# Optimization experiments

Measured on AMD Instinct MI355X. Metric: run time of the kernel, lower is better.

Reference implementation:

```python
import jax, jax.numpy as jnp
import numpy as np

B, S, D, H = 2, 2048, 1024, 16
DH = D // H
DIM_K = 1024


def setup_inputs() -> dict:
    key = jax.random.key(0)
    ks = jax.random.split(key, 5)
    sc = 0.02
    return {
        "x": jax.random.normal(ks[0], (B, S, D), dtype=jnp.float32),
        "Wq": jax.random.normal(ks[1], (D, DIM_K), dtype=jnp.float32) * sc,
        "Wk": jax.random.normal(ks[2], (D, DIM_K), dtype=jnp.float32) * sc,
        "Wv": jax.random.normal(ks[3], (D, DIM_K), dtype=jnp.float32) * sc,
        "Wo": jax.random.normal(ks[4], (DIM_K, DIM_K), dtype=jnp.float32) * sc,
    }


def reference(x, Wq, Wk, Wv, Wo):
    # projections (Linear, no bias); weights stored as [in, out]
    q = (x @ Wq).reshape(B, S, H, DH).transpose(0, 2, 1, 3)  # [B,H,S,DH]
    k = (x @ Wk).reshape(B, S, H, DH).transpose(0, 2, 1, 3)
    v = (x @ Wv).reshape(B, S, H, DH).transpose(0, 2, 1, 3)

    scores = jnp.einsum("bhqd,bhkd->bhqk", q, k)  # [B,H,S,S]
    # causal mask applied BEFORE scaling, as in the original
    causal_mask = jnp.triu(jnp.ones((S, S), dtype=bool), k=1)
    m_inf = -jnp.finfo(scores.dtype).max
    scores = jnp.where(causal_mask[None, None], m_inf, scores)
    attn = jax.nn.softmax(scores * (DIM_K ** -0.5), axis=-1)

    out = jnp.einsum("bhqk,bhkd->bhqd", attn, v)  # [B,H,S,DH]
    out = out.transpose(0, 2, 1, 3).reshape(B, S, DIM_K)
    return out @ Wo
```

## Files before the change

### kernel.cpp

```cpp
#include <hip/hip_runtime.h>


#define AS1 __attribute__((address_space(1)))
#define AS3 __attribute__((address_space(3)))
#define EXPC2 0.04508422f

typedef __attribute__((ext_vector_type(4))) float f32x4;
typedef __attribute__((ext_vector_type(8))) short bf16x8;

__device__ __forceinline__ void gload16(const void* g, void* l) {
  __builtin_amdgcn_global_load_lds((const AS1 unsigned int*)g,
                                   (AS3 unsigned int*)l, 16, 0, 0);
}
__device__ __forceinline__ unsigned short f2b(float f) {
  unsigned u = __float_as_uint(f);
  return (unsigned short)((u + 0x7FFFu + ((u >> 16) & 1u)) >> 16);
}
__device__ __forceinline__ float fexp2(float x) {
  float r;
  asm("v_exp_f32 %0, %1" : "=v"(r) : "v"(x));
  return r;
}
__device__ __forceinline__ unsigned cvtpk(float a, float b) {
  unsigned r;
  asm("v_cvt_pk_bf16_f32 %0, %1, %2" : "=v"(r) : "v"(a), "v"(b));
  return r;
}

__global__ __launch_bounds__(256) void prep(
    const float* __restrict__ x, const float* __restrict__ W0,
    const float* __restrict__ W1, const float* __restrict__ W2,
    const float* __restrict__ W3, unsigned short* __restrict__ xb,
    unsigned short* __restrict__ Wt) {
  __shared__ float T[64][65];
  const int tid = threadIdx.x;
  const int bid = blockIdx.x;
  if (bid < 4096) {
    const size_t i = (size_t)(bid * 256 + tid) * 4;
    float4 v = *(const float4*)&x[i];
    uint2 o;
    o.x = f2b(v.x) | ((unsigned)f2b(v.y) << 16);
    o.y = f2b(v.z) | ((unsigned)f2b(v.w) << 16);
    *(uint2*)&xb[i] = o;
    return;
  }
  const int idx = bid - 4096;
  const int kb = (idx & 15) * 64, nb = ((idx >> 4) & 15) * 64, z = idx >> 8;
  const float* W = (z == 0) ? W0 : (z == 1) ? W1 : (z == 2) ? W2 : W3;
  unsigned short* D = Wt + (size_t)z * 1024 * 1024;
#pragma unroll
  for (int p = 0; p < 4; ++p) {
    const int s = p * 256 + tid;
    const int r = s >> 4, c4 = s & 15;
    float4 v = *(const float4*)&W[(size_t)(kb + r) * 1024 + nb + c4 * 4];
    T[r][c4 * 4 + 0] = v.x;
    T[r][c4 * 4 + 1] = v.y;
    T[r][c4 * 4 + 2] = v.z;
    T[r][c4 * 4 + 3] = v.w;
  }
  __syncthreads();
#pragma unroll
  for (int p = 0; p < 4; ++p) {
    const int s = p * 256 + tid;
    const int n = s >> 4, k4 = s & 15;
    uint2 o;
    o.x = f2b(T[k4 * 4 + 0][n]) | ((unsigned)f2b(T[k4 * 4 + 1][n]) << 16);
    o.y = f2b(T[k4 * 4 + 2][n]) | ((unsigned)f2b(T[k4 * 4 + 3][n]) << 16);
    *(uint2*)&D[(size_t)(nb + n) * 1024 + kb + k4 * 4] = o;
  }
}

template <int KIND>
__global__ __launch_bounds__(256) void gemm2ph(
    const unsigned short* __restrict__ A, const unsigned short* __restrict__ B,
    unsigned short* __restrict__ Qb, unsigned short* __restrict__ Kb,
    unsigned short* __restrict__ Vp, float* __restrict__ Of) {
  __shared__ unsigned short smem[16896];

  const int tid = threadIdx.x, lane = tid & 63, w = tid >> 6;
  int bm, bn;
  if constexpr (KIND == 0) {
    bm = blockIdx.x / 24;
    bn = blockIdx.x % 24;
  } else {
    bm = blockIdx.x >> 3;
    bn = blockIdx.x & 7;
  }
  const int wr = w >> 1, wc = w & 1;

  f32x4 acc[4][4];
#pragma unroll
  for (int m = 0; m < 4; ++m)
#pragma unroll
    for (int n = 0; n < 4; ++n) acc[m][n] = (f32x4)0.0f;

  const int lu = (lane & 7) ^ (lane >> 3);
  const int srow2 = 2 * (lane >> 3) + (lu >> 2);
  const int scol2 = (lu & 3) * 8;
  const size_t arow = (size_t)(bm * 128 + srow2) * 1024 + scol2;
  const size_t brow = (size_t)(bn * 128 + srow2) * 1024 + scol2;

  const int fr = lane & 15, g = lane >> 4;
  const int fh = fr >> 1;
  const int pcx = ((((fr & 1) << 2) | g) ^ fh) * 8;

#define GSTAGE(BUF, KC)                                                      \
  {                                                                          \
    _Pragma("unroll") for (int q = 0; q < 2; ++q) {                          \
      const int r = w * 32 + q * 16;                                         \
      gload16(&A[arow + (size_t)r * 1024 + (KC)],                            \
              &smem[(BUF) * 8192 + r * 32]);                                 \
      gload16(&B[brow + (size_t)r * 1024 + (KC)],                            \
              &smem[(BUF) * 8192 + 4096 + r * 32]);                          \
    }                                                                        \
  }

  GSTAGE(0, 0)
  int cur = 0;

  for (int t = 0; t < 32; ++t) {
    __syncthreads();
    if (t + 1 < 32) GSTAGE(cur ^ 1, (t + 1) * 32)

    bf16x8 af[4], bf[4];
#pragma unroll
    for (int m = 0; m < 4; ++m)
      af[m] = *(const bf16x8*)&smem[cur * 8192 + (wr * 32 + m * 8 + fh) * 64 +
                                    pcx];
#pragma unroll
    for (int n = 0; n < 4; ++n)
      bf[n] = *(const bf16x8*)&smem[cur * 8192 + 4096 +
                                    (wc * 32 + n * 8 + fh) * 64 + pcx];
#pragma unroll
    for (int m = 0; m < 4; ++m)
#pragma unroll
      for (int n = 0; n < 4; ++n)
        acc[m][n] = __builtin_amdgcn_mfma_f32_16x16x32_bf16(af[m], bf[n],
                                                            acc[m][n], 0, 0, 0);
    cur ^= 1;
  }

  const int fq = lane >> 4;
  if constexpr (KIND == 1) {
#pragma unroll
    for (int mf = 0; mf < 4; ++mf)
#pragma unroll
      for (int nf = 0; nf < 4; ++nf) {
        const int col = bn * 128 + wc * 64 + nf * 16 + fr;
#pragma unroll
        for (int rr = 0; rr < 4; ++rr) {
          const int m = bm * 128 + wr * 64 + mf * 16 + fq * 4 + rr;
          Of[(size_t)m * 1024 + col] = acc[mf][nf][rr];
        }
      }
    return;
  } else if (bn < 16) {
    unsigned short* Ob = (bn < 8) ? Qb : Kb;
    const int cbase = (bn & 7) * 128;
#pragma unroll
    for (int mf = 0; mf < 4; ++mf)
#pragma unroll
      for (int nf = 0; nf < 4; ++nf) {
        const int col = cbase + wc * 64 + nf * 16 + fr;
        const int h = col >> 6, d = col & 63;
#pragma unroll
        for (int rr = 0; rr < 4; ++rr) {
          const int m = bm * 128 + wr * 64 + mf * 16 + fq * 4 + rr;
          const int b = m >> 11, s = m & 2047;
          Ob[((size_t)(b * 16 + h) * 2048 + s) * 64 + d] = f2b(acc[mf][nf][rr]);
        }
      }
    return;
  }

  __syncthreads();
#pragma unroll
  for (int mf = 0; mf < 4; ++mf)
#pragma unroll
    for (int nf = 0; nf < 4; ++nf) {
      const int cl = wc * 64 + nf * 16 + fr;
#pragma unroll
      for (int rr = 0; rr < 4; ++rr) {
        const int ml = wr * 64 + mf * 16 + fq * 4 + rr;
        const int u = ml & 63, a = u >> 4;
        const int sperm = (ml & 64) | ((a >> 1) * 32 + ((u >> 2) & 3) * 8 +
                                       (a & 1) * 4 + (u & 3));
        smem[cl * 132 + sperm] = f2b(acc[mf][nf][rr]);
      }
    }
  __syncthreads();
  const int l5 = lane & 31;
  const size_t sbase = (size_t)((bm * 128) & 2047);
  const int bV = bm >> 4;
#pragma unroll
  for (int it = 0; it < 16; ++it) {
    const int rl = w * 32 + it * 2 + (lane >> 5);
    const int rowg = (bn - 16) * 128 + rl;
    const int h = rowg >> 6, d = rowg & 63;
    uint2 v = *(const uint2*)&smem[rl * 132 + l5 * 4];
    *(uint2*)&Vp[((size_t)(bV * 16 + h) * 64 + d) * 2048 + sbase + l5 * 4] = v;
  }
#undef GSTAGE
}

__global__ __launch_bounds__(256) void attn_q64(
    const unsigned short* __restrict__ Qb, const unsigned short* __restrict__ Kb,
    const unsigned short* __restrict__ Vp, unsigned short* __restrict__ Ab) {
  __shared__ unsigned short smem[16384];

  const int tid = threadIdx.x, lane = tid & 63, w = tid >> 6;
  const int lo = lane & 15, hi = lane >> 4;

  const int id = blockIdx.x;
  const int qtr = id >> 8;
  const int g = (id >> 5) & 7;
  const int bh = id & 31;
  const int bq = (qtr == 0)   ? 2 * g
                 : (qtr == 1) ? 2 * g + 1
                 : (qtr == 2) ? 31 - 2 * g
                              : 30 - 2 * g;
  const int qw = bq * 64 + w * 16;
  const size_t base = (size_t)bh * (2048 * 64);

  bf16x8 qf[2];
#pragma unroll
  for (int ks = 0; ks < 2; ++ks)
    qf[ks] =
        *(const bf16x8*)&Qb[base + (size_t)(qw + lo) * 64 + ks * 32 + hi * 8];

  f32x4 accO[4];
#pragma unroll
  for (int mf = 0; mf < 4; ++mf) accO[mf] = (f32x4)0.0f;
  float mrow = -1e30f, lpart = 0.0f;

  const int ntile = bq + 1;
  const unsigned short* kgb = Kb + base;
  const unsigned short* vgb = Vp + base;
  const int lseg = w * 512;

#define STAGE(BUF, KBASE)                                                    \
  {                                                                          \
    const int kb_ = (KBASE);                                                 \
    _Pragma("unroll") for (int qq = 0; qq < 2; ++qq) {                       \
      const int slot = qq * 256 + tid;                                       \
      const int row = slot >> 3, ch = (slot & 7) ^ (row & 7);                \
      gload16(kgb + (size_t)(kb_ + row) * 64 + ch * 8,                       \
              &smem[(BUF)*4096 + qq * 2048 + lseg]);                         \
      gload16(vgb + (size_t)row * 2048 + kb_ + ch * 8,                       \
              &smem[8192 + (BUF)*4096 + qq * 2048 + lseg]);                  \
    }                                                                        \
  }

  STAGE(0, 0)
  int cur = 0;

  for (int t = 0; t < ntile; ++t) {
    __syncthreads();
    if (t + 1 < ntile) STAGE(cur ^ 1, (t + 1) * 64)

    const int kb = t * 64;
    const int x7 = lo & 7;
    bf16x8 ka[2][4];
#pragma unroll
    for (int ks = 0; ks < 2; ++ks) {
      const int ch = (ks * 4 + hi) ^ x7;
#pragma unroll
      for (int kf = 0; kf < 4; ++kf)
        ka[ks][kf] =
            *(const bf16x8*)&smem[cur * 4096 + (kf * 16 + lo) * 64 + ch * 8];
    }
    f32x4 st[4];
#pragma unroll
    for (int kf = 0; kf < 4; ++kf) st[kf] = (f32x4)0.0f;
    __builtin_amdgcn_s_setprio(1);
#pragma unroll
    for (int ks = 0; ks < 2; ++ks)
#pragma unroll
      for (int kf = 0; kf < 4; ++kf)
        st[kf] = __builtin_amdgcn_mfma_f32_16x16x32_bf16(ka[ks][kf], qf[ks],
                                                         st[kf], 0, 0, 0);
    __builtin_amdgcn_s_setprio(0);

    bf16x8 va[2][4];
#pragma unroll
    for (int ks = 0; ks < 2; ++ks) {
      const int ch = (ks * 4 + hi) ^ x7;
#pragma unroll
      for (int mf = 0; mf < 4; ++mf)
        va[ks][mf] = *(const bf16x8*)&smem[8192 + cur * 4096 +
                                           (mf * 16 + lo) * 64 + ch * 8];
    }

    float v[16];
#pragma unroll
    for (int kf = 0; kf < 4; ++kf)
#pragma unroll
      for (int rr = 0; rr < 4; ++rr) v[kf * 4 + rr] = st[kf][rr];
    if (kb + 63 > qw) {
      const int qg = qw + lo;
#pragma unroll
      for (int kf = 0; kf < 4; ++kf)
#pragma unroll
        for (int rr = 0; rr < 4; ++rr)
          if (kb + kf * 16 + hi * 4 + rr > qg) v[kf * 4 + rr] = -1e30f;
    }
    float mx = fmaxf(fmaxf(fmaxf(v[0], v[1]), fmaxf(v[2], v[3])),
                     fmaxf(fmaxf(v[4], v[5]), fmaxf(v[6], v[7])));
    mx = fmaxf(mx, fmaxf(fmaxf(fmaxf(v[8], v[9]), fmaxf(v[10], v[11])),
                         fmaxf(fmaxf(v[12], v[13]), fmaxf(v[14], v[15]))));
    mx = fmaxf(mx, __shfl_xor(mx, 16));
    mx = fmaxf(mx, __shfl_xor(mx, 32));
    if (!__all(mx - mrow <= 64.0f)) {
      const float mnew = fmaxf(mrow, mx);
      const float al = fexp2((mrow - mnew) * EXPC2);
      mrow = mnew;
      lpart *= al;
#pragma unroll
      for (int mf = 0; mf < 4; ++mf)
#pragma unroll
        for (int rr = 0; rr < 4; ++rr) accO[mf][rr] *= al;
    }
    float p[16], rs = 0.0f;
#pragma unroll
    for (int i = 0; i < 16; ++i) {
      p[i] = fexp2((v[i] - mrow) * EXPC2);
      rs += p[i];
    }
    lpart += rs;

    bf16x8 pb[2];
#pragma unroll
    for (int ks = 0; ks < 2; ++ks) {
      uint4 u;
      u.x = cvtpk(p[ks * 8 + 0], p[ks * 8 + 1]);
      u.y = cvtpk(p[ks * 8 + 2], p[ks * 8 + 3]);
      u.z = cvtpk(p[ks * 8 + 4], p[ks * 8 + 5]);
      u.w = cvtpk(p[ks * 8 + 6], p[ks * 8 + 7]);
      pb[ks] = *(bf16x8*)&u;
    }

    __builtin_amdgcn_s_setprio(1);
#pragma unroll
    for (int ks = 0; ks < 2; ++ks)
#pragma unroll
      for (int mf = 0; mf < 4; ++mf)
        accO[mf] = __builtin_amdgcn_mfma_f32_16x16x32_bf16(va[ks][mf], pb[ks],
                                                           accO[mf], 0, 0, 0);
    __builtin_amdgcn_s_setprio(0);
    cur ^= 1;
  }

  __syncthreads();

  float l = lpart;
  l += __shfl_xor(l, 16);
  l += __shfl_xor(l, 32);
  const float linv = 1.0f / l;
  unsigned short* ot = &smem[w * 1152];
#pragma unroll
  for (int mf = 0; mf < 4; ++mf) {
    uint2 u;
    u.x = cvtpk(accO[mf][0] * linv, accO[mf][1] * linv);
    u.y = cvtpk(accO[mf][2] * linv, accO[mf][3] * linv);
    *(uint2*)&ot[lo * 72 + mf * 16 + hi * 4] = u;
  }
  const int b = bh >> 4, h = bh & 15;
  const int row = lane >> 2, cg = (lane & 3) * 16;
  uint4 o0 = *(const uint4*)&ot[row * 72 + cg];
  uint4 o1 = *(const uint4*)&ot[row * 72 + cg + 8];
  unsigned short* op = &Ab[(size_t)(b * 2048 + qw + row) * 1024 + h * 64 + cg];
  *(uint4*)op = o0;
  *(uint4*)(op + 8) = o1;
}

extern "C" void kernel_launch(void* const* d_in, const int* in_sizes, int n_in,
                              void* d_out, int out_size, void* d_ws,
                              size_t ws_size, hipStream_t stream) {
  (void)in_sizes; (void)n_in; (void)out_size; (void)ws_size;
  const float* x = (const float*)d_in[0];
  const float* Wq = (const float*)d_in[1];
  const float* Wk = (const float*)d_in[2];
  const float* Wv = (const float*)d_in[3];
  const float* Wo = (const float*)d_in[4];
  float* out = (float*)d_out;

  char* ws = (char*)d_ws;
  unsigned short* xb = (unsigned short*)(ws);
  unsigned short* Wt = (unsigned short*)(ws + (8u << 20));
  unsigned short* Qb = (unsigned short*)(ws + (16u << 20));
  unsigned short* Kb = (unsigned short*)(ws + (24u << 20));
  unsigned short* Vp = (unsigned short*)(ws + (32u << 20));
  unsigned short* Ab = (unsigned short*)(ws + (40u << 20));
  unsigned short* Wto = Wt + (size_t)3 * 1024 * 1024;

  prep<<<dim3(5120), 256, 0, stream>>>(x, Wq, Wk, Wv, Wo, xb, Wt);
  gemm2ph<0><<<dim3(768), 256, 0, stream>>>(xb, Wt, Qb, Kb, Vp, nullptr);
  attn_q64<<<dim3(1024), 256, 0, stream>>>(Qb, Kb, Vp, Ab);
  gemm2ph<1><<<dim3(256), 256, 0, stream>>>(Ab, Wto, nullptr, nullptr, nullptr,
                                            out);
}
```

Measured before the change: 111.8 us.

## Drop LDS staging in attention and GEMM A operand, load fragments from global

The attention kernel no longer stages K/V tiles through shared memory. Each wave loads its K and V MFMA fragments straight from global memory, double-buffering K in registers. It now covers 32 query rows per wave in two 16-row halves, and blocks are remapped so each XCD handles a fixed set of heads, with half as many blocks launched. The projection GEMM also loads its A fragments directly from global into registers with register double-buffering, and only B goes through LDS. This removes LDS traffic and barriers but relies on cache hits for data shared across waves, and raises register pressure.

```diff
diff --git a/kernel.cpp b/kernel.cpp
--- a/kernel.cpp
+++ b/kernel.cpp
@@ -97,47 +97,49 @@
   const int lu = (lane & 7) ^ (lane >> 3);
   const int srow2 = 2 * (lane >> 3) + (lu >> 2);
   const int scol2 = (lu & 3) * 8;
-  const size_t arow = (size_t)(bm * 128 + srow2) * 1024 + scol2;
   const size_t brow = (size_t)(bn * 128 + srow2) * 1024 + scol2;
 
   const int fr = lane & 15, g = lane >> 4;
   const int fh = fr >> 1;
   const int pcx = ((((fr & 1) << 2) | g) ^ fh) * 8;
+
+  const size_t aFragBase = (size_t)(bm * 128 + wr * 64 + fr) * 1024 + g * 8;
+  bf16x8 afA[4], afB[4];
+#pragma unroll
+  for (int m = 0; m < 4; ++m)
+    afA[m] = *(const bf16x8*)&A[aFragBase + (size_t)m * 16384];
 
 #define GSTAGE(BUF, KC)                                                      \
   {                                                                          \
     _Pragma("unroll") for (int q = 0; q < 2; ++q) {                          \
       const int r = w * 32 + q * 16;                                         \
-      gload16(&A[arow + (size_t)r * 1024 + (KC)],                            \
-              &smem[(BUF) * 8192 + r * 32]);                                 \
       gload16(&B[brow + (size_t)r * 1024 + (KC)],                            \
-              &smem[(BUF) * 8192 + 4096 + r * 32]);                          \
+              &smem[(BUF) * 4096 + r * 32]);                                 \
     }                                                                        \
   }
 
+#define GSTEP(T, AC, AN)                                                     \
+  {                                                                          \
+    __syncthreads();          \
+    if ((T) + 1 < 32) {                                                      \
+      GSTAGE(((T) + 1) & 1, ((T) + 1) * 32)                                  \
+      _Pragma("unroll") for (int m = 0; m < 4; ++m) AN[m] =                  \
+          *(const bf16x8*)&A[aFragBase + (size_t)m * 16384 + ((T) + 1) * 32];\
+    }                                                                        \
+    bf16x8 bf[4];                                                            \
+    _Pragma("unroll") for (int n = 0; n < 4; ++n) bf[n] =                    \
+        *(const bf16x8*)&smem[((T)&1) * 4096 + (wc * 32 + n * 8 + fh) * 64 + \
+                              pcx];                                          \
+    _Pragma("unroll") for (int m = 0; m < 4; ++m)                            \
+        _Pragma("unroll") for (int n = 0; n < 4; ++n) acc[m][n] =            \
+            __builtin_amdgcn_mfma_f32_16x16x32_bf16(AC[m], bf[n], acc[m][n], \
+                                                    0, 0, 0);                \
+  }
+
   GSTAGE(0, 0)
-  int cur = 0;
-
-  for (int t = 0; t < 32; ++t) {
-    __syncthreads();
-    if (t + 1 < 32) GSTAGE(cur ^ 1, (t + 1) * 32)
-
-    bf16x8 af[4], bf[4];
-#pragma unroll
-    for (int m = 0; m < 4; ++m)
-      af[m] = *(const bf16x8*)&smem[cur * 8192 + (wr * 32 + m * 8 + fh) * 64 +
-                                    pcx];
-#pragma unroll
-    for (int n = 0; n < 4; ++n)
-      bf[n] = *(const bf16x8*)&smem[cur * 8192 + 4096 +
-                                    (wc * 32 + n * 8 + fh) * 64 + pcx];
-#pragma unroll
-    for (int m = 0; m < 4; ++m)
-#pragma unroll
-      for (int n = 0; n < 4; ++n)
-        acc[m][n] = __builtin_amdgcn_mfma_f32_16x16x32_bf16(af[m], bf[n],
-                                                            acc[m][n], 0, 0, 0);
-    cur ^= 1;
+  for (int t = 0; t < 32; t += 2) {
+    GSTEP(t, afA, afB)
+    GSTEP(t + 1, afB, afA)
   }
 
   const int fq = lane >> 4;
@@ -200,177 +202,149 @@
     uint2 v = *(const uint2*)&smem[rl * 132 + l5 * 4];
     *(uint2*)&Vp[((size_t)(bV * 16 + h) * 64 + d) * 2048 + sbase + l5 * 4] = v;
   }
+#undef GSTEP
 #undef GSTAGE
 }
 
-__global__ __launch_bounds__(256) void attn_q64(
+__global__ __launch_bounds__(256) void attn_nolds(
     const unsigned short* __restrict__ Qb, const unsigned short* __restrict__ Kb,
     const unsigned short* __restrict__ Vp, unsigned short* __restrict__ Ab) {
-  __shared__ unsigned short smem[16384];
-
   const int tid = threadIdx.x, lane = tid & 63, w = tid >> 6;
   const int lo = lane & 15, hi = lane >> 4;
 
   const int id = blockIdx.x;
-  const int qtr = id >> 8;
-  const int g = (id >> 5) & 7;
-  const int bh = id & 31;
-  const int bq = (qtr == 0)   ? 2 * g
-                 : (qtr == 1) ? 2 * g + 1
-                 : (qtr == 2) ? 31 - 2 * g
-                              : 30 - 2 * g;
-  const int qw = bq * 64 + w * 16;
+  const int xcd = id & 7, mm = id >> 3;
+  const int bh = xcd * 4 + (mm & 3);
+  const int h8 = mm >> 2;
+  const int bq4 = (h8 < 8) ? h8 : 23 - h8;
+  const int t32 = bq4 * 4 + w;
+  const int qw = t32 * 32;
+  const int ntile = (t32 >> 1) + 1;
   const size_t base = (size_t)bh * (2048 * 64);
-
-  bf16x8 qf[2];
-#pragma unroll
-  for (int ks = 0; ks < 2; ++ks)
-    qf[ks] =
-        *(const bf16x8*)&Qb[base + (size_t)(qw + lo) * 64 + ks * 32 + hi * 8];
-
-  f32x4 accO[4];
-#pragma unroll
-  for (int mf = 0; mf < 4; ++mf) accO[mf] = (f32x4)0.0f;
-  float mrow = -1e30f, lpart = 0.0f;
-
-  const int ntile = bq + 1;
-  const unsigned short* kgb = Kb + base;
-  const unsigned short* vgb = Vp + base;
-  const int lseg = w * 512;
-
-#define STAGE(BUF, KBASE)                                                    \
+  const unsigned short* kg = Kb + base;
+  const unsigned short* vg = Vp + base;
+
+  bf16x8 qf[2][2];
+#pragma unroll
+  for (int qn = 0; qn < 2; ++qn)
+#pragma unroll
+    for (int ks = 0; ks < 2; ++ks)
+      qf[qn][ks] = *(const bf16x8*)&Qb[base +
+                                       (size_t)(qw + qn * 16 + lo) * 64 +
+                                       ks * 32 + hi * 8];
+
+  f32x4 accO[4][2];
+#pragma unroll
+  for (int mf = 0; mf < 4; ++mf)
+#pragma unroll
+    for (int qn = 0; qn < 2; ++qn) accO[mf][qn] = (f32x4)0.0f;
+  float mrow[2] = {-1e30f, -1e30f}, lpart[2] = {0.0f, 0.0f};
+
+  bf16x8 kaA[2][4], kaB[2][4];
+#define LOADK(DST, KB_)                                                      \
+  _Pragma("unroll") for (int ks = 0; ks < 2; ++ks)                           \
+      _Pragma("unroll") for (int kf = 0; kf < 4; ++kf) DST[ks][kf] =         \
+          *(const bf16x8*)&kg[(size_t)((KB_) + kf * 16 + lo) * 64 +          \
+                              ks * 32 + hi * 8];
+
+#define ATILE(T, KA, KN)                                                     \
   {                                                                          \
-    const int kb_ = (KBASE);                                                 \
-    _Pragma("unroll") for (int qq = 0; qq < 2; ++qq) {                       \
-      const int slot = qq * 256 + tid;                                       \
-      const int row = slot >> 3, ch = (slot & 7) ^ (row & 7);                \
-      gload16(kgb + (size_t)(kb_ + row) * 64 + ch * 8,                       \
-              &smem[(BUF)*4096 + qq * 2048 + lseg]);                         \
-      gload16(vgb + (size_t)row * 2048 + kb_ + ch * 8,                       \
-              &smem[8192 + (BUF)*4096 + qq * 2048 + lseg]);                  \
+    const int kb = (T) * 64;                                                 \
+    f32x4 st[4][2];                                                          \
+    _Pragma("unroll") for (int kf = 0; kf < 4; ++kf)                         \
+        _Pragma("unroll") for (int qn = 0; qn < 2; ++qn) st[kf][qn] =        \
+            (f32x4)0.0f;                                                     \
+    __builtin_amdgcn_s_setprio(1);                                           \
+    _Pragma("unroll") for (int ks = 0; ks < 2; ++ks)                         \
+        _Pragma("unroll") for (int kf = 0; kf < 4; ++kf)                     \
+            _Pragma("unroll") for (int qn = 0; qn < 2; ++qn) st[kf][qn] =    \
+                __builtin_amdgcn_mfma_f32_16x16x32_bf16(                     \
+                    KA[ks][kf], qf[qn][ks], st[kf][qn], 0, 0, 0);            \
+    __builtin_amdgcn_s_setprio(0);                                           \
+    if ((T) + 1 < ntile) LOADK(KN, ((T) + 1) * 64)                           \
+    bf16x8 va[2][4];    \
+    _Pragma("unroll") for (int ks = 0; ks < 2; ++ks)                         \
+        _Pragma("unroll") for (int mf = 0; mf < 4; ++mf) va[ks][mf] =        \
+            *(const bf16x8*)&vg[(size_t)(mf * 16 + lo) * 2048 + kb +         \
+                                ks * 32 + hi * 8];                           \
+    bf16x8 pb[2][2];                                                         \
+    _Pragma("unroll") for (int qn = 0; qn < 2; ++qn) {                       \
+      float v[16];                                                           \
+      _Pragma("unroll") for (int kf = 0; kf < 4; ++kf)                       \
+          _Pragma("unroll") for (int rr = 0; rr < 4; ++rr) v[kf * 4 + rr] =  \
+              st[kf][qn][rr];                                                \
+      if (kb + 63 > qw) {                                                    \
+        const int qg = qw + qn * 16 + lo;                                    \
+        _Pragma("unroll") for (int kf = 0; kf < 4; ++kf)                     \
+            _Pragma("unroll") for (int rr = 0; rr < 4; ++rr) if (kb +        \
+                kf * 16 + hi * 4 + rr > qg) v[kf * 4 + rr] = -1e30f;         \
+      }                                                                      \
+      float mx = fmaxf(fmaxf(fmaxf(v[0], v[1]), fmaxf(v[2], v[3])),          \
+                       fmaxf(fmaxf(v[4], v[5]), fmaxf(v[6], v[7])));         \
+      mx = fmaxf(mx, fmaxf(fmaxf(fmaxf(v[8], v[9]), fmaxf(v[10], v[11])),    \
+                           fmaxf(fmaxf(v[12], v[13]), fmaxf(v[14], v[15]))));\
+      mx = fmaxf(mx, __shfl_xor(mx, 16));                                    \
+      mx = fmaxf(mx, __shfl_xor(mx, 32));                                    \
+      if (!__all(mx - mrow[qn] <= 64.0f)) {           \
+        const float mnew = fmaxf(mrow[qn], mx);                              \
+        const float al = fexp2((mrow[qn] - mnew) * EXPC2);                   \
+        mrow[qn] = mnew;                                                     \
+        lpart[qn] *= al;                                                     \
+        _Pragma("unroll") for (int mf = 0; mf < 4; ++mf)                     \
+            _Pragma("unroll") for (int rr = 0; rr < 4; ++rr)                 \
+                accO[mf][qn][rr] *= al;                                      \
+      }                                                                      \
+      float p[16], rs = 0.0f;                                                \
+      _Pragma("unroll") for (int i = 0; i < 16; ++i) {                       \
+        p[i] = fexp2((v[i] - mrow[qn]) * EXPC2);                             \
+        rs += p[i];                                                          \
+      }                                                                      \
+      lpart[qn] += rs;                                                       \
+      _Pragma("unroll") for (int ks = 0; ks < 2; ++ks) {                     \
+        uint4 u;                                                             \
+        u.x = cvtpk(p[ks * 8 + 0], p[ks * 8 + 1]);                           \
+        u.y = cvtpk(p[ks * 8 + 2], p[ks * 8 + 3]);                           \
+        u.z = cvtpk(p[ks * 8 + 4], p[ks * 8 + 5]);                           \
+        u.w = cvtpk(p[ks * 8 + 6], p[ks * 8 + 7]);                           \
+        pb[qn][ks] = *(bf16x8*)&u;                                           \
+      }                                                                      \
     }                                                                        \
-  }
-
-  STAGE(0, 0)
-  int cur = 0;
-
-  for (int t = 0; t < ntile; ++t) {
-    __syncthreads();
-    if (t + 1 < ntile) STAGE(cur ^ 1, (t + 1) * 64)
-
-    const int kb = t * 64;
-    const int x7 = lo & 7;
-    bf16x8 ka[2][4];
-#pragma unroll
-    for (int ks = 0; ks < 2; ++ks) {
-      const int ch = (ks * 4 + hi) ^ x7;
-#pragma unroll
-      for (int kf = 0; kf < 4; ++kf)
-        ka[ks][kf] =
-            *(const bf16x8*)&smem[cur * 4096 + (kf * 16 + lo) * 64 + ch * 8];
+    __builtin_amdgcn_s_setprio(1);                                           \
+    _Pragma("unroll") for (int ks = 0; ks < 2; ++ks)                         \
+        _Pragma("unroll") for (int mf = 0; mf < 4; ++mf)                     \
+            _Pragma("unroll") for (int qn = 0; qn < 2; ++qn) accO[mf][qn] =  \
+                __builtin_amdgcn_mfma_f32_16x16x32_bf16(                     \
+                    va[ks][mf], pb[qn][ks], accO[mf][qn], 0, 0, 0);          \
+    __builtin_amdgcn_s_setprio(0);                                           \
+  }
+
+  LOADK(kaA, 0)
+  int t = 0;
+  while (true) {
+    ATILE(t, kaA, kaB)
+    if (++t >= ntile) break;
+    ATILE(t, kaB, kaA)
+    if (++t >= ntile) break;
+  }
+
+  const int b = bh >> 4, h = bh & 15;
+#pragma unroll
+  for (int qn = 0; qn < 2; ++qn) {
+    float l = lpart[qn];
+    l += __shfl_xor(l, 16);
+    l += __shfl_xor(l, 32);
+    const float linv = 1.0f / l;
+#pragma unroll
+    for (int mf = 0; mf < 4; ++mf) {
+      uint2 u;
+      u.x = cvtpk(accO[mf][qn][0] * linv, accO[mf][qn][1] * linv);
+      u.y = cvtpk(accO[mf][qn][2] * linv, accO[mf][qn][3] * linv);
+      *(uint2*)&Ab[(size_t)(b * 2048 + qw + qn * 16 + lo) * 1024 + h * 64 +
+                   mf * 16 + hi * 4] = u;
     }
-    f32x4 st[4];
-#pragma unroll
-    for (int kf = 0; kf < 4; ++kf) st[kf] = (f32x4)0.0f;
-    __builtin_amdgcn_s_setprio(1);
-#pragma unroll
-    for (int ks = 0; ks < 2; ++ks)
-#pragma unroll
-      for (int kf = 0; kf < 4; ++kf)
-        st[kf] = __builtin_amdgcn_mfma_f32_16x16x32_bf16(ka[ks][kf], qf[ks],
-                                                         st[kf], 0, 0, 0);
-    __builtin_amdgcn_s_setprio(0);
-
-    bf16x8 va[2][4];
-#pragma unroll
-    for (int ks = 0; ks < 2; ++ks) {
-      const int ch = (ks * 4 + hi) ^ x7;
-#pragma unroll
-      for (int mf = 0; mf < 4; ++mf)
-        va[ks][mf] = *(const bf16x8*)&smem[8192 + cur * 4096 +
-                                           (mf * 16 + lo) * 64 + ch * 8];
-    }
-
-    float v[16];
-#pragma unroll
-    for (int kf = 0; kf < 4; ++kf)
-#pragma unroll
-      for (int rr = 0; rr < 4; ++rr) v[kf * 4 + rr] = st[kf][rr];
-    if (kb + 63 > qw) {
-      const int qg = qw + lo;
-#pragma unroll
-      for (int kf = 0; kf < 4; ++kf)
-#pragma unroll
-        for (int rr = 0; rr < 4; ++rr)
-          if (kb + kf * 16 + hi * 4 + rr > qg) v[kf * 4 + rr] = -1e30f;
-    }
-    float mx = fmaxf(fmaxf(fmaxf(v[0], v[1]), fmaxf(v[2], v[3])),
-                     fmaxf(fmaxf(v[4], v[5]), fmaxf(v[6], v[7])));
-    mx = fmaxf(mx, fmaxf(fmaxf(fmaxf(v[8], v[9]), fmaxf(v[10], v[11])),
-                         fmaxf(fmaxf(v[12], v[13]), fmaxf(v[14], v[15]))));
-    mx = fmaxf(mx, __shfl_xor(mx, 16));
-    mx = fmaxf(mx, __shfl_xor(mx, 32));
-    if (!__all(mx - mrow <= 64.0f)) {
-      const float mnew = fmaxf(mrow, mx);
-      const float al = fexp2((mrow - mnew) * EXPC2);
-      mrow = mnew;
-      lpart *= al;
-#pragma unroll
-      for (int mf = 0; mf < 4; ++mf)
-#pragma unroll
-        for (int rr = 0; rr < 4; ++rr) accO[mf][rr] *= al;
-    }
-    float p[16], rs = 0.0f;
-#pragma unroll
-    for (int i = 0; i < 16; ++i) {
-      p[i] = fexp2((v[i] - mrow) * EXPC2);
-      rs += p[i];
-    }
-    lpart += rs;
-
-    bf16x8 pb[2];
-#pragma unroll
-    for (int ks = 0; ks < 2; ++ks) {
-      uint4 u;
-      u.x = cvtpk(p[ks * 8 + 0], p[ks * 8 + 1]);
-      u.y = cvtpk(p[ks * 8 + 2], p[ks * 8 + 3]);
-      u.z = cvtpk(p[ks * 8 + 4], p[ks * 8 + 5]);
-      u.w = cvtpk(p[ks * 8 + 6], p[ks * 8 + 7]);
-      pb[ks] = *(bf16x8*)&u;
-    }
-
-    __builtin_amdgcn_s_setprio(1);
-#pragma unroll
-    for (int ks = 0; ks < 2; ++ks)
-#pragma unroll
-      for (int mf = 0; mf < 4; ++mf)
-        accO[mf] = __builtin_amdgcn_mfma_f32_16x16x32_bf16(va[ks][mf], pb[ks],
-                                                           accO[mf], 0, 0, 0);
-    __builtin_amdgcn_s_setprio(0);
-    cur ^= 1;
-  }
-
-  __syncthreads();
-
-  float l = lpart;
-  l += __shfl_xor(l, 16);
-  l += __shfl_xor(l, 32);
-  const float linv = 1.0f / l;
-  unsigned short* ot = &smem[w * 1152];
-#pragma unroll
-  for (int mf = 0; mf < 4; ++mf) {
-    uint2 u;
-    u.x = cvtpk(accO[mf][0] * linv, accO[mf][1] * linv);
-    u.y = cvtpk(accO[mf][2] * linv, accO[mf][3] * linv);
-    *(uint2*)&ot[lo * 72 + mf * 16 + hi * 4] = u;
-  }
-  const int b = bh >> 4, h = bh & 15;
-  const int row = lane >> 2, cg = (lane & 3) * 16;
-  uint4 o0 = *(const uint4*)&ot[row * 72 + cg];
-  uint4 o1 = *(const uint4*)&ot[row * 72 + cg + 8];
-  unsigned short* op = &Ab[(size_t)(b * 2048 + qw + row) * 1024 + h * 64 + cg];
-  *(uint4*)op = o0;
-  *(uint4*)(op + 8) = o1;
+  }
+#undef ATILE
+#undef LOADK
 }
 
 extern "C" void kernel_launch(void* const* d_in, const int* in_sizes, int n_in,
@@ -395,7 +369,7 @@
 
   prep<<<dim3(5120), 256, 0, stream>>>(x, Wq, Wk, Wv, Wo, xb, Wt);
   gemm2ph<0><<<dim3(768), 256, 0, stream>>>(xb, Wt, Qb, Kb, Vp, nullptr);
-  attn_q64<<<dim3(1024), 256, 0, stream>>>(Qb, Kb, Vp, Ab);
+  attn_nolds<<<dim3(512), 256, 0, stream>>>(Qb, Kb, Vp, Ab);
   gemm2ph<1><<<dim3(256), 256, 0, stream>>>(Ab, Wto, nullptr, nullptr, nullptr,
                                             out);
 }
```

Measured after the change: 179.3 us. +60.5%, slower.

## Split attention across block-tiled kernel and new single-wave register kernel per batch

Applied to the files above, without the earlier changes.

The existing LDS-based attention kernel now handles only the first 16 batch-head pairs. A new single-wave kernel, which reads K and V straight from global memory into registers with double-buffered K fragments, handles the other 16. Each wave computes 32 query rows, and the heaviest tiles are scheduled first. The goal is to try a different occupancy and memory-access structure, but the two kernels run serially on the same stream, and the new one gives up LDS reuse across waves.

```diff
diff --git a/kernel.cpp b/kernel.cpp
--- a/kernel.cpp
+++ b/kernel.cpp
@@ -212,9 +212,9 @@
   const int lo = lane & 15, hi = lane >> 4;
 
   const int id = blockIdx.x;
-  const int qtr = id >> 8;
-  const int g = (id >> 5) & 7;
-  const int bh = id & 31;
+  const int qtr = id >> 7;
+  const int g = (id >> 4) & 7;
+  const int bh = id & 15;
   const int bq = (qtr == 0)   ? 2 * g
                  : (qtr == 1) ? 2 * g + 1
                  : (qtr == 2) ? 31 - 2 * g
@@ -371,6 +371,145 @@
   unsigned short* op = &Ab[(size_t)(b * 2048 + qw + row) * 1024 + h * 64 + cg];
   *(uint4*)op = o0;
   *(uint4*)(op + 8) = o1;
+#undef STAGE
+}
+
+__global__ __launch_bounds__(64) void attn_wave(
+    const unsigned short* __restrict__ Qb, const unsigned short* __restrict__ Kb,
+    const unsigned short* __restrict__ Vp, unsigned short* __restrict__ Ab) {
+  const int lane = threadIdx.x & 63;
+  const int lo = lane & 15, hi = lane >> 4;
+
+  const int id = blockIdx.x;
+  const int bh = 16 + (id & 15);
+  const int t32 = 63 - (id >> 4);
+  const int qw = t32 * 32;
+  const int ntile = (t32 >> 1) + 1;
+  const size_t base = (size_t)bh * (2048 * 64);
+  const unsigned short* kg = Kb + base;
+  const unsigned short* vg = Vp + base;
+
+  bf16x8 qf[2][2];
+#pragma unroll
+  for (int qn = 0; qn < 2; ++qn)
+#pragma unroll
+    for (int ks = 0; ks < 2; ++ks)
+      qf[qn][ks] = *(const bf16x8*)&Qb[base +
+                                       (size_t)(qw + qn * 16 + lo) * 64 +
+                                       ks * 32 + hi * 8];
+
+  f32x4 accO[4][2];
+#pragma unroll
+  for (int mf = 0; mf < 4; ++mf)
+#pragma unroll
+    for (int qn = 0; qn < 2; ++qn) accO[mf][qn] = (f32x4)0.0f;
+  float mrow[2] = {-1e30f, -1e30f}, lpart[2] = {0.0f, 0.0f};
+
+  bf16x8 kaA[2][4], kaB[2][4];
+#define LOADK(DST, KB_)                                                      \
+  _Pragma("unroll") for (int ks = 0; ks < 2; ++ks)                           \
+      _Pragma("unroll") for (int kf = 0; kf < 4; ++kf) DST[ks][kf] =         \
+          *(const bf16x8*)&kg[(size_t)((KB_) + kf * 16 + lo) * 64 +          \
+                              ks * 32 + hi * 8];
+
+#define ATILE(T, KA, KN)                                                     \
+  {                                                                          \
+    const int kb = (T) * 64;                                                 \
+    f32x4 st[4][2];                                                          \
+    _Pragma("unroll") for (int kf = 0; kf < 4; ++kf)                         \
+        _Pragma("unroll") for (int qn = 0; qn < 2; ++qn) st[kf][qn] =        \
+            (f32x4)0.0f;                                                     \
+    __builtin_amdgcn_s_setprio(1);                                           \
+    _Pragma("unroll") for (int ks = 0; ks < 2; ++ks)                         \
+        _Pragma("unroll") for (int kf = 0; kf < 4; ++kf)                     \
+            _Pragma("unroll") for (int qn = 0; qn < 2; ++qn) st[kf][qn] =    \
+                __builtin_amdgcn_mfma_f32_16x16x32_bf16(                     \
+                    KA[ks][kf], qf[qn][ks], st[kf][qn], 0, 0, 0);            \
+    __builtin_amdgcn_s_setprio(0);                                           \
+    if ((T) + 1 < ntile) LOADK(KN, ((T) + 1) * 64)                           \
+    bf16x8 va[2][4];                                                         \
+    _Pragma("unroll") for (int ks = 0; ks < 2; ++ks)                         \
+        _Pragma("unroll") for (int mf = 0; mf < 4; ++mf) va[ks][mf] =        \
+            *(const bf16x8*)&vg[(size_t)(mf * 16 + lo) * 2048 + kb +         \
+                                ks * 32 + hi * 8];                           \
+    bf16x8 pb[2][2];                                                         \
+    _Pragma("unroll") for (int qn = 0; qn < 2; ++qn) {                       \
+      float v[16];                                                           \
+      _Pragma("unroll") for (int kf = 0; kf < 4; ++kf)                       \
+          _Pragma("unroll") for (int rr = 0; rr < 4; ++rr) v[kf * 4 + rr] =  \
+              st[kf][qn][rr];                                                \
+      if (kb + 63 > qw) {                                                    \
+        const int qg = qw + qn * 16 + lo;                                    \
+        _Pragma("unroll") for (int kf = 0; kf < 4; ++kf)                     \
+            _Pragma("unroll") for (int rr = 0; rr < 4; ++rr) if (kb +        \
+                kf * 16 + hi * 4 + rr > qg) v[kf * 4 + rr] = -1e30f;         \
+      }                                                                      \
+      float mx = fmaxf(fmaxf(fmaxf(v[0], v[1]), fmaxf(v[2], v[3])),          \
+                       fmaxf(fmaxf(v[4], v[5]), fmaxf(v[6], v[7])));         \
+      mx = fmaxf(mx, fmaxf(fmaxf(fmaxf(v[8], v[9]), fmaxf(v[10], v[11])),    \
+                           fmaxf(fmaxf(v[12], v[13]), fmaxf(v[14], v[15]))));\
+      mx = fmaxf(mx, __shfl_xor(mx, 16));                                    \
+      mx = fmaxf(mx, __shfl_xor(mx, 32));                                    \
+      if (!__all(mx - mrow[qn] <= 64.0f)) {                                  \
+        const float mnew = fmaxf(mrow[qn], mx);                              \
+        const float al = fexp2((mrow[qn] - mnew) * EXPC2);                   \
+        mrow[qn] = mnew;                                                     \
+        lpart[qn] *= al;                                                     \
+        _Pragma("unroll") for (int mf = 0; mf < 4; ++mf)                     \
+            _Pragma("unroll") for (int rr = 0; rr < 4; ++rr)                 \
+                accO[mf][qn][rr] *= al;                                      \
+      }                                                                      \
+      float p[16], rs = 0.0f;                                                \
+      _Pragma("unroll") for (int i = 0; i < 16; ++i) {                       \
+        p[i] = fexp2((v[i] - mrow[qn]) * EXPC2);                             \
+        rs += p[i];                                                          \
+      }                                                                      \
+      lpart[qn] += rs;                                                       \
+      _Pragma("unroll") for (int ks = 0; ks < 2; ++ks) {                     \
+        uint4 u;                                                             \
+        u.x = cvtpk(p[ks * 8 + 0], p[ks * 8 + 1]);                           \
+        u.y = cvtpk(p[ks * 8 + 2], p[ks * 8 + 3]);                           \
+        u.z = cvtpk(p[ks * 8 + 4], p[ks * 8 + 5]);                           \
+        u.w = cvtpk(p[ks * 8 + 6], p[ks * 8 + 7]);                           \
+        pb[qn][ks] = *(bf16x8*)&u;                                           \
+      }                                                                      \
+    }                                                                        \
+    __builtin_amdgcn_s_setprio(1);                                           \
+    _Pragma("unroll") for (int ks = 0; ks < 2; ++ks)                         \
+        _Pragma("unroll") for (int mf = 0; mf < 4; ++mf)                     \
+            _Pragma("unroll") for (int qn = 0; qn < 2; ++qn) accO[mf][qn] =  \
+                __builtin_amdgcn_mfma_f32_16x16x32_bf16(                     \
+                    va[ks][mf], pb[qn][ks], accO[mf][qn], 0, 0, 0);          \
+    __builtin_amdgcn_s_setprio(0);                                           \
+  }
+
+  LOADK(kaA, 0)
+  int t = 0;
+  while (true) {
+    ATILE(t, kaA, kaB)
+    if (++t >= ntile) break;
+    ATILE(t, kaB, kaA)
+    if (++t >= ntile) break;
+  }
+
+  const int b = bh >> 4, h = bh & 15;
+#pragma unroll
+  for (int qn = 0; qn < 2; ++qn) {
+    float l = lpart[qn];
+    l += __shfl_xor(l, 16);
+    l += __shfl_xor(l, 32);
+    const float linv = 1.0f / l;
+#pragma unroll
+    for (int mf = 0; mf < 4; ++mf) {
+      uint2 u;
+      u.x = cvtpk(accO[mf][qn][0] * linv, accO[mf][qn][1] * linv);
+      u.y = cvtpk(accO[mf][qn][2] * linv, accO[mf][qn][3] * linv);
+      *(uint2*)&Ab[(size_t)(b * 2048 + qw + qn * 16 + lo) * 1024 + h * 64 +
+                   mf * 16 + hi * 4] = u;
+    }
+  }
+#undef ATILE
+#undef LOADK
 }
 
 extern "C" void kernel_launch(void* const* d_in, const int* in_sizes, int n_in,
@@ -395,7 +534,8 @@
 
   prep<<<dim3(5120), 256, 0, stream>>>(x, Wq, Wk, Wv, Wo, xb, Wt);
   gemm2ph<0><<<dim3(768), 256, 0, stream>>>(xb, Wt, Qb, Kb, Vp, nullptr);
-  attn_q64<<<dim3(1024), 256, 0, stream>>>(Qb, Kb, Vp, Ab);
+  attn_q64<<<dim3(512), 256, 0, stream>>>(Qb, Kb, Vp, Ab);
+  attn_wave<<<dim3(1024), 64, 0, stream>>>(Qb, Kb, Vp, Ab);
   gemm2ph<1><<<dim3(256), 256, 0, stream>>>(Ab, Wto, nullptr, nullptr, nullptr,
                                             out);
 }
```

Result: slower. 146.9 us (+31.5%).

## Enlarge QKV projection GEMM tile to 256x256 with 512-thread blocks

Applied to the files above, without the earlier changes.

Splits the shared GEMM into a dedicated QKV kernel with 256x256 output tiles computed by 8 waves of 64x128 each, and a separate output-projection GEMM that keeps the old 128x128 tiling. Larger tiles raise operand reuse from LDS and halve global loads per FLOP. The V-transposed epilogue is staged through shared memory in four quadrant passes. The trade-off is only 192 blocks for 256 CUs, plus higher register pressure from the doubled accumulator count.

```diff
diff --git a/kernel.cpp b/kernel.cpp
--- a/kernel.cpp
+++ b/kernel.cpp
@@ -70,22 +70,132 @@
   }
 }
 
-template <int KIND>
-__global__ __launch_bounds__(256) void gemm2ph(
+__global__ __launch_bounds__(512, 2) void gemm_qkv(
+    const unsigned short* __restrict__ xb, const unsigned short* __restrict__ Wt,
+    unsigned short* __restrict__ Qb, unsigned short* __restrict__ Kb,
+    unsigned short* __restrict__ Vp) {
+  __shared__ unsigned short smem[32768];
+
+  const int tid = threadIdx.x, lane = tid & 63, w = tid >> 6;
+  const int bm = blockIdx.x / 12, bn = blockIdx.x % 12;
+  const int wr = w >> 1, wc = w & 1;
+
+  f32x4 acc[4][8];
+#pragma unroll
+  for (int m = 0; m < 4; ++m)
+#pragma unroll
+    for (int n = 0; n < 8; ++n) acc[m][n] = (f32x4)0.0f;
+
+  const int lu = (lane & 7) ^ (lane >> 3);
+  const int srow2 = 2 * (lane >> 3) + (lu >> 2);
+  const int scol2 = (lu & 3) * 8;
+  const int c0 = w * 2, c1 = w * 2 + 1;
+  const size_t arow0 = (size_t)(bm * 256 + c0 * 16 + srow2) * 1024 + scol2;
+  const size_t arow1 = (size_t)(bm * 256 + c1 * 16 + srow2) * 1024 + scol2;
+  const size_t brow0 = (size_t)(bn * 256 + c0 * 16 + srow2) * 1024 + scol2;
+  const size_t brow1 = (size_t)(bn * 256 + c1 * 16 + srow2) * 1024 + scol2;
+
+  const int fr = lane & 15, g = lane >> 4;
+  const int fh = fr >> 1;
+  const int pcx = ((((fr & 1) << 2) | g) ^ fh) * 8;
+
+#define QSTAGE(BUF, KC)                                                      \
+  {                                                                          \
+    gload16(&xb[arow0 + (KC)], &smem[(BUF)*16384 + c0 * 512]);               \
+    gload16(&xb[arow1 + (KC)], &smem[(BUF)*16384 + c1 * 512]);               \
+    gload16(&Wt[brow0 + (KC)], &smem[8192 + (BUF)*16384 + c0 * 512]);        \
+    gload16(&Wt[brow1 + (KC)], &smem[8192 + (BUF)*16384 + c1 * 512]);        \
+  }
+
+  QSTAGE(0, 0)
+  int cur = 0;
+
+  for (int t = 0; t < 32; ++t) {
+    __syncthreads();
+    if (t + 1 < 32) QSTAGE(cur ^ 1, (t + 1) * 32)
+
+    bf16x8 af[4], bf[8];
+#pragma unroll
+    for (int m = 0; m < 4; ++m)
+      af[m] = *(const bf16x8*)&smem[cur * 16384 + (wr * 32 + m * 8 + fh) * 64 +
+                                    pcx];
+#pragma unroll
+    for (int n = 0; n < 8; ++n)
+      bf[n] = *(const bf16x8*)&smem[8192 + cur * 16384 +
+                                    (wc * 64 + n * 8 + fh) * 64 + pcx];
+#pragma unroll
+    for (int m = 0; m < 4; ++m)
+#pragma unroll
+      for (int n = 0; n < 8; ++n)
+        acc[m][n] = __builtin_amdgcn_mfma_f32_16x16x32_bf16(af[m], bf[n],
+                                                            acc[m][n], 0, 0, 0);
+    cur ^= 1;
+  }
+
+  const int fq = lane >> 4;
+  if (bn < 8) {
+    unsigned short* Ob = (bn < 4) ? Qb : Kb;
+    const int cbase = (bn & 3) * 256;
+#pragma unroll
+    for (int mf = 0; mf < 4; ++mf)
+#pragma unroll
+      for (int nf = 0; nf < 8; ++nf) {
+        const int col = cbase + wc * 128 + nf * 16 + fr;
+        const int h = col >> 6, d = col & 63;
+#pragma unroll
+        for (int rr = 0; rr < 4; ++rr) {
+          const int m = bm * 256 + wr * 64 + mf * 16 + fq * 4 + rr;
+          const int b = m >> 11, s = m & 2047;
+          Ob[((size_t)(b * 16 + h) * 2048 + s) * 64 + d] = f2b(acc[mf][nf][rr]);
+        }
+      }
+    return;
+  }
+
+  const int chb = (bn - 8) * 256;
+  const int s0all = bm * 256;
+  const int b = s0all >> 11;
+#pragma unroll
+  for (int qq = 0; qq < 4; ++qq) {
+    const int qm = qq >> 1, qn = qq & 1;
+    __syncthreads();
+    if (wc == qn && (wr >> 1) == qm) {
+#pragma unroll
+      for (int mf = 0; mf < 4; ++mf)
+#pragma unroll
+        for (int nf = 0; nf < 8; ++nf) {
+          const int cl = nf * 16 + fr;
+#pragma unroll
+          for (int rr = 0; rr < 4; ++rr) {
+            const int ml = (wr & 1) * 64 + mf * 16 + fq * 4 + rr;
+            const int u = ml & 63, a = u >> 4;
+            const int sperm = (ml & 64) | ((a >> 1) * 32 + ((u >> 2) & 3) * 8 +
+                                           (a & 1) * 4 + (u & 3));
+            smem[cl * 132 + sperm] = f2b(acc[mf][nf][rr]);
+          }
+        }
+    }
+    __syncthreads();
+    const int row = tid >> 2, cg = (tid & 3) * 32;
+    const int ch = chb + qn * 128 + row;
+    const int h = ch >> 6, d = ch & 63;
+    const int sb = (s0all + qm * 128) & 2047;
+    unsigned short* dst = &Vp[((size_t)(b * 16 + h) * 64 + d) * 2048 + sb + cg];
+    *(uint4*)(dst + 0) = *(const uint4*)&smem[row * 132 + cg];
+    *(uint4*)(dst + 8) = *(const uint4*)&smem[row * 132 + cg + 8];
+    *(uint4*)(dst + 16) = *(const uint4*)&smem[row * 132 + cg + 16];
+    *(uint4*)(dst + 24) = *(const uint4*)&smem[row * 132 + cg + 24];
+  }
+#undef QSTAGE
+}
+
+__global__ __launch_bounds__(256) void gemm_out(
     const unsigned short* __restrict__ A, const unsigned short* __restrict__ B,
-    unsigned short* __restrict__ Qb, unsigned short* __restrict__ Kb,
-    unsigned short* __restrict__ Vp, float* __restrict__ Of) {
-  __shared__ unsigned short smem[16896];
+    float* __restrict__ Of) {
+  __shared__ unsigned short smem[16384];
 
   const int tid = threadIdx.x, lane = tid & 63, w = tid >> 6;
-  int bm, bn;
-  if constexpr (KIND == 0) {
-    bm = blockIdx.x / 24;
-    bn = blockIdx.x % 24;
-  } else {
-    bm = blockIdx.x >> 3;
-    bn = blockIdx.x & 7;
-  }
+  const int bm = blockIdx.x >> 3, bn = blockIdx.x & 7;
   const int wr = w >> 1, wc = w & 1;
 
   f32x4 acc[4][4];
@@ -104,7 +214,7 @@
   const int fh = fr >> 1;
   const int pcx = ((((fr & 1) << 2) | g) ^ fh) * 8;
 
-#define GSTAGE(BUF, KC)                                                      \
+#define OSTAGE(BUF, KC)                                                      \
   {                                                                          \
     _Pragma("unroll") for (int q = 0; q < 2; ++q) {                          \
       const int r = w * 32 + q * 16;                                         \
@@ -115,12 +225,12 @@
     }                                                                        \
   }
 
-  GSTAGE(0, 0)
+  OSTAGE(0, 0)
   int cur = 0;
 
   for (int t = 0; t < 32; ++t) {
     __syncthreads();
-    if (t + 1 < 32) GSTAGE(cur ^ 1, (t + 1) * 32)
+    if (t + 1 < 32) OSTAGE(cur ^ 1, (t + 1) * 32)
 
     bf16x8 af[4], bf[4];
 #pragma unroll
@@ -141,66 +251,18 @@
   }
 
   const int fq = lane >> 4;
-  if constexpr (KIND == 1) {
-#pragma unroll
-    for (int mf = 0; mf < 4; ++mf)
-#pragma unroll
-      for (int nf = 0; nf < 4; ++nf) {
-        const int col = bn * 128 + wc * 64 + nf * 16 + fr;
-#pragma unroll
-        for (int rr = 0; rr < 4; ++rr) {
-          const int m = bm * 128 + wr * 64 + mf * 16 + fq * 4 + rr;
-          Of[(size_t)m * 1024 + col] = acc[mf][nf][rr];
-        }
+#pragma unroll
+  for (int mf = 0; mf < 4; ++mf)
+#pragma unroll
+    for (int nf = 0; nf < 4; ++nf) {
+      const int col = bn * 128 + wc * 64 + nf * 16 + fr;
+#pragma unroll
+      for (int rr = 0; rr < 4; ++rr) {
+        const int m = bm * 128 + wr * 64 + mf * 16 + fq * 4 + rr;
+        Of[(size_t)m * 1024 + col] = acc[mf][nf][rr];
       }
-    return;
-  } else if (bn < 16) {
-    unsigned short* Ob = (bn < 8) ? Qb : Kb;
-    const int cbase = (bn & 7) * 128;
-#pragma unroll
-    for (int mf = 0; mf < 4; ++mf)
-#pragma unroll
-      for (int nf = 0; nf < 4; ++nf) {
-        const int col = cbase + wc * 64 + nf * 16 + fr;
-        const int h = col >> 6, d = col & 63;
-#pragma unroll
-        for (int rr = 0; rr < 4; ++rr) {
-          const int m = bm * 128 + wr * 64 + mf * 16 + fq * 4 + rr;
-          const int b = m >> 11, s = m & 2047;
-          Ob[((size_t)(b * 16 + h) * 2048 + s) * 64 + d] = f2b(acc[mf][nf][rr]);
-        }
-      }
-    return;
-  }
-
-  __syncthreads();
-#pragma unroll
-  for (int mf = 0; mf < 4; ++mf)
-#pragma unroll
-    for (int nf = 0; nf < 4; ++nf) {
-      const int cl = wc * 64 + nf * 16 + fr;
-#pragma unroll
-      for (int rr = 0; rr < 4; ++rr) {
-        const int ml = wr * 64 + mf * 16 + fq * 4 + rr;
-        const int u = ml & 63, a = u >> 4;
-        const int sperm = (ml & 64) | ((a >> 1) * 32 + ((u >> 2) & 3) * 8 +
-                                       (a & 1) * 4 + (u & 3));
-        smem[cl * 132 + sperm] = f2b(acc[mf][nf][rr]);
-      }
-    }
-  __syncthreads();
-  const int l5 = lane & 31;
-  const size_t sbase = (size_t)((bm * 128) & 2047);
-  const int bV = bm >> 4;
-#pragma unroll
-  for (int it = 0; it < 16; ++it) {
-    const int rl = w * 32 + it * 2 + (lane >> 5);
-    const int rowg = (bn - 16) * 128 + rl;
-    const int h = rowg >> 6, d = rowg & 63;
-    uint2 v = *(const uint2*)&smem[rl * 132 + l5 * 4];
-    *(uint2*)&Vp[((size_t)(bV * 16 + h) * 64 + d) * 2048 + sbase + l5 * 4] = v;
-  }
-#undef GSTAGE
+    }
+#undef OSTAGE
 }
 
 __global__ __launch_bounds__(256) void attn_q64(
@@ -371,6 +433,7 @@
   unsigned short* op = &Ab[(size_t)(b * 2048 + qw + row) * 1024 + h * 64 + cg];
   *(uint4*)op = o0;
   *(uint4*)(op + 8) = o1;
+#undef STAGE
 }
 
 extern "C" void kernel_launch(void* const* d_in, const int* in_sizes, int n_in,
@@ -394,8 +457,7 @@
   unsigned short* Wto = Wt + (size_t)3 * 1024 * 1024;
 
   prep<<<dim3(5120), 256, 0, stream>>>(x, Wq, Wk, Wv, Wo, xb, Wt);
-  gemm2ph<0><<<dim3(768), 256, 0, stream>>>(xb, Wt, Qb, Kb, Vp, nullptr);
+  gemm_qkv<<<dim3(192), 512, 0, stream>>>(xb, Wt, Qb, Kb, Vp);
   attn_q64<<<dim3(1024), 256, 0, stream>>>(Qb, Kb, Vp, Ab);
-  gemm2ph<1><<<dim3(256), 256, 0, stream>>>(Ab, Wto, nullptr, nullptr, nullptr,
-                                            out);
-}
+  gemm_out<<<dim3(256), 256, 0, stream>>>(Ab, Wto, out);
+}
```

Measured after the change: 108.1 us. -3.3%, faster.
